# Kernel optimization log

Hardware: AMD Instinct MI355X
Metric: run time of the kernel (lower is better)

Reference implementation:

```python
import jax, jax.numpy as jnp
import numpy as np

D_MODEL = 1024
NUM_HEADS = 16
HEAD_DIM = D_MODEL // NUM_HEADS
FFN_HIDDEN = 4096
EPS = 1e-5


def setup_inputs() -> dict:
    key = jax.random.key(0)
    ks = jax.random.split(key, 7)
    s = 0.02
    return {
        "x": jax.random.normal(ks[0], (2, 2048, D_MODEL), dtype=jnp.float32),
        "W_qkv": jax.random.normal(ks[1], (D_MODEL, 3 * D_MODEL), dtype=jnp.float32) * s,
        "b_qkv": jnp.zeros((3 * D_MODEL,), dtype=jnp.float32),
        "W_o": jax.random.normal(ks[2], (D_MODEL, D_MODEL), dtype=jnp.float32) * s,
        "b_o": jnp.zeros((D_MODEL,), dtype=jnp.float32),
        "gamma1": jnp.ones((D_MODEL,), dtype=jnp.float32),
        "beta1": jnp.zeros((D_MODEL,), dtype=jnp.float32),
        "W1": jax.random.normal(ks[3], (D_MODEL, FFN_HIDDEN), dtype=jnp.float32) * s,
        "b1": jnp.zeros((FFN_HIDDEN,), dtype=jnp.float32),
        "W2": jax.random.normal(ks[4], (FFN_HIDDEN, D_MODEL), dtype=jnp.float32) * s,
        "b2": jnp.zeros((D_MODEL,), dtype=jnp.float32),
        "gamma2": jnp.ones((D_MODEL,), dtype=jnp.float32),
        "beta2": jnp.zeros((D_MODEL,), dtype=jnp.float32),
    }


def _layernorm(x, gamma, beta):
    mean = jnp.mean(x, axis=-1, keepdims=True)
    var = jnp.mean((x - mean) ** 2, axis=-1, keepdims=True)
    return gamma * (x - mean) / jnp.sqrt(var + EPS) + beta


def reference(x, W_qkv, b_qkv, W_o, b_o, gamma1, beta1, W1, b1, W2, b2, gamma2, beta2):
    B, S, D = x.shape
    # ---- multi-head attention ----
    qkv = x @ W_qkv + b_qkv                       # [B,S,3D]
    qkv = qkv.reshape(B, S, NUM_HEADS, 3 * HEAD_DIM).transpose(0, 2, 1, 3)  # [B,H,S,3hd]
    q, k, v = jnp.split(qkv, 3, axis=-1)          # each [B,H,S,hd]
    scores = jnp.einsum("bhqd,bhkd->bhqk", q, k) / np.sqrt(HEAD_DIM)
    attn = jax.nn.softmax(scores, axis=-1)
    vals = jnp.einsum("bhqk,bhkd->bhqd", attn, v)
    vals = vals.transpose(0, 2, 1, 3).reshape(B, S, D)
    attn_out = vals @ W_o + b_o
    # dropout disabled (eval mode)
    h = _layernorm(attn_out + x, gamma1, beta1)
    # ---- position-wise FFN (dropout before relu per source, disabled) ----
    ffn = jax.nn.relu(h @ W1 + b1) @ W2 + b2
    return _layernorm(ffn + h, gamma2, beta2)
```

## Files before the change

### kernel.cpp

```cpp
#include <hip/hip_runtime.h>
#include <stdint.h>

typedef float v4f __attribute__((ext_vector_type(4)));
typedef __bf16 v8bf __attribute__((ext_vector_type(8)));
typedef __bf16 v4bf __attribute__((ext_vector_type(4)));
typedef unsigned short v8us __attribute__((ext_vector_type(8)));
typedef unsigned short v4us __attribute__((ext_vector_type(4)));

__device__ __forceinline__ float b2f(unsigned short u) {
    union { float f; uint32_t i; } x; x.i = ((uint32_t)u) << 16; return x.f;
}
__device__ __forceinline__ unsigned short f2b(float f) {
    union { float f; uint32_t u; } x; x.f = f;
    uint32_t r = x.u + 0x7fffu + ((x.u >> 16) & 1u);
    return (unsigned short)(r >> 16);
}

__device__ __forceinline__ void gload16(const unsigned short* g, unsigned short* l) {
    __builtin_amdgcn_global_load_lds(
        (const __attribute__((address_space(1))) void*)g,
        (__attribute__((address_space(3))) void*)l,
        16, 0, 0);
}

__global__ __launch_bounds__(256) void convert_f32_bf16(
    const float* __restrict__ src, unsigned short* __restrict__ dst)
{
    int i = (blockIdx.x * 256 + threadIdx.x) * 4;
    float4 v = *(const float4*)&src[i];
    v4us o = {f2b(v.x), f2b(v.y), f2b(v.z), f2b(v.w)};
    *(v4us*)&dst[i] = o;
}

__global__ __launch_bounds__(256) void transpose_to_bt(
    const float* __restrict__ W, unsigned short* __restrict__ WT, int K, int N)
{
    __shared__ unsigned short t[64][65];
    const int kb = blockIdx.y * 64, nb = blockIdx.x * 64;
    const int r = threadIdx.x >> 4, c4 = (threadIdx.x & 15) * 4;
    #pragma unroll
    for (int i = 0; i < 4; ++i) {
        int k = r + i * 16;
        float4 v = *(const float4*)&W[(size_t)(kb + k) * N + nb + c4];
        t[c4 + 0][k] = f2b(v.x);
        t[c4 + 1][k] = f2b(v.y);
        t[c4 + 2][k] = f2b(v.z);
        t[c4 + 3][k] = f2b(v.w);
    }
    __syncthreads();
    #pragma unroll
    for (int i = 0; i < 4; ++i) {
        int n = r + i * 16;
        v4us o = {t[n][c4], t[n][c4 + 1], t[n][c4 + 2], t[n][c4 + 3]};
        *(v4us*)&WT[(size_t)(nb + n) * K + kb + c4] = o;
    }
}

__device__ __forceinline__ void xcd_swizzle(int& bm, int& bn) {
    int NB = gridDim.x, MB = gridDim.y;
    int flat = blockIdx.x + NB * blockIdx.y;
    int xcd = flat & 7, j = flat >> 3;
    int MBand = MB >> 3;
    bm = xcd * MBand + (j % MBand);
    bn = j / MBand;
}

template<int SPLIT_V>
__global__ __launch_bounds__(256) void gemm_bt(
    const unsigned short* __restrict__ A, const unsigned short* __restrict__ BT,
    const float* __restrict__ bias, unsigned short* __restrict__ C,
    unsigned short* __restrict__ VT, int M, int N, int K, int relu)
{
    __shared__ __align__(16) unsigned short sA[2][128 * 32];
    __shared__ __align__(16) unsigned short sB[2][128 * 32];
    const int tid  = threadIdx.x;
    const int wave = tid >> 6, lane = tid & 63;
    const int wm = wave >> 1, wn = wave & 1;
    const int quad = lane >> 4, l16 = lane & 15;
    int bm, bn;
    xcd_swizzle(bm, bn);

    const int srow = lane >> 2, scol = (lane & 3) * 8;
    const unsigned short* ga0 = A  + (size_t)(bm * 128 + (wave * 2 + 0) * 16 + srow) * K + scol;
    const unsigned short* ga1 = A  + (size_t)(bm * 128 + (wave * 2 + 1) * 16 + srow) * K + scol;
    const unsigned short* gb0 = BT + (size_t)(bn * 128 + (wave * 2 + 0) * 16 + srow) * K + scol;
    const unsigned short* gb1 = BT + (size_t)(bn * 128 + (wave * 2 + 1) * 16 + srow) * K + scol;
    const int o0 = (wave * 2 + 0) * 512 + lane * 8;
    const int o1 = (wave * 2 + 1) * 512 + lane * 8;

    v8us aR[2][2], bR[2][2];
    #pragma unroll
    for (int c = 0; c < 2; ++c) {
        aR[c][0] = *(const v8us*)(ga0 + c * 32);
        aR[c][1] = *(const v8us*)(ga1 + c * 32);
        bR[c][0] = *(const v8us*)(gb0 + c * 32);
        bR[c][1] = *(const v8us*)(gb1 + c * 32);
    }

    v4f acc[4][4];
    #pragma unroll
    for (int i = 0; i < 4; ++i)
        #pragma unroll
        for (int j = 0; j < 4; ++j)
            acc[i][j] = (v4f){0.f, 0.f, 0.f, 0.f};

    for (int kt = 0; kt < K; kt += 64) {
        __syncthreads();
        #pragma unroll
        for (int c = 0; c < 2; ++c) {
            *(v8us*)&sA[c][o0] = aR[c][0];
            *(v8us*)&sA[c][o1] = aR[c][1];
            *(v8us*)&sB[c][o0] = bR[c][0];
            *(v8us*)&sB[c][o1] = bR[c][1];
        }
        __syncthreads();
        if (kt + 64 < K) {
            int kn = kt + 64;
            #pragma unroll
            for (int c = 0; c < 2; ++c) {
                aR[c][0] = *(const v8us*)(ga0 + kn + c * 32);
                aR[c][1] = *(const v8us*)(ga1 + kn + c * 32);
                bR[c][0] = *(const v8us*)(gb0 + kn + c * 32);
                bR[c][1] = *(const v8us*)(gb1 + kn + c * 32);
            }
        }

        #pragma unroll
        for (int c = 0; c < 2; ++c) {
            v8bf af[4], bfr[4];
            #pragma unroll
            for (int mt = 0; mt < 4; ++mt)
                af[mt] = *(const v8bf*)&sA[c][(wm * 64 + mt * 16 + l16) * 32 + quad * 8];
            #pragma unroll
            for (int nt = 0; nt < 4; ++nt)
                bfr[nt] = *(const v8bf*)&sB[c][(wn * 64 + nt * 16 + l16) * 32 + quad * 8];
            #pragma unroll
            for (int mt = 0; mt < 4; ++mt)
                #pragma unroll
                for (int nt = 0; nt < 4; ++nt)
                    acc[mt][nt] = __builtin_amdgcn_mfma_f32_16x16x32_bf16(
                        af[mt], bfr[nt], acc[mt][nt], 0, 0, 0);
        }
    }

    #pragma unroll
    for (int mt = 0; mt < 4; ++mt) {
        int row = bm * 128 + wm * 64 + mt * 16 + quad * 4;
        #pragma unroll
        for (int nt = 0; nt < 4; ++nt) {
            int c0 = bn * 128 + wn * 64 + nt * 16;
            int col = c0 + l16;
            float bv = bias ? bias[col] : 0.f;
            if (SPLIT_V && (c0 % 192) >= 128) {
                int hh = c0 / 192;
                int d  = (c0 % 192) - 128 + l16;
                int bb = row >> 11;
                int s  = row & 2047;
                v4us st;
                #pragma unroll
                for (int r = 0; r < 4; ++r)
                    st[r] = f2b(acc[mt][nt][r] + bv);
                *(v4us*)&VT[((size_t)(bb * 16 + hh) * 64 + d) * 2048 + s] = st;
            } else {
                float qs = (SPLIT_V && (c0 % 192) < 64) ? 0.18033688f : 1.0f;
                #pragma unroll
                for (int r = 0; r < 4; ++r) {
                    float v = (acc[mt][nt][r] + bv) * qs;
                    if (relu) v = fmaxf(v, 0.f);
                    C[(size_t)(row + r) * N + col] = f2b(v);
                }
            }
        }
    }
}

__global__ __launch_bounds__(256) void gemm_bt_n64(
    const unsigned short* __restrict__ A, const unsigned short* __restrict__ BT,
    const float* __restrict__ bias, unsigned short* __restrict__ C,
    int M, int N, int K, int relu)
{
    __shared__ __align__(16) unsigned short sA[2][128 * 32];
    __shared__ __align__(16) unsigned short sB[2][64 * 32];
    const int tid  = threadIdx.x;
    const int wave = tid >> 6, lane = tid & 63;
    const int wm = wave >> 1, wn = wave & 1;
    const int quad = lane >> 4, l16 = lane & 15;
    int bm, bn;
    xcd_swizzle(bm, bn);

    const int srow = lane >> 2, scol = (lane & 3) * 8;
    const unsigned short* ga0 = A  + (size_t)(bm * 128 + (wave * 2 + 0) * 16 + srow) * K + scol;
    const unsigned short* ga1 = A  + (size_t)(bm * 128 + (wave * 2 + 1) * 16 + srow) * K + scol;
    const unsigned short* gb0 = BT + (size_t)(bn * 64 + wave * 16 + srow) * K + scol;
    const int oa0 = (wave * 2 + 0) * 512 + lane * 8;
    const int oa1 = (wave * 2 + 1) * 512 + lane * 8;
    const int ob  = wave * 512 + lane * 8;

    v8us aR[2][2], bR[2];
    #pragma unroll
    for (int c = 0; c < 2; ++c) {
        aR[c][0] = *(const v8us*)(ga0 + c * 32);
        aR[c][1] = *(const v8us*)(ga1 + c * 32);
        bR[c]    = *(const v8us*)(gb0 + c * 32);
    }

    v4f acc[4][2];
    #pragma unroll
    for (int i = 0; i < 4; ++i)
        #pragma unroll
        for (int j = 0; j < 2; ++j)
            acc[i][j] = (v4f){0.f, 0.f, 0.f, 0.f};

    for (int kt = 0; kt < K; kt += 64) {
        __syncthreads();
        #pragma unroll
        for (int c = 0; c < 2; ++c) {
            *(v8us*)&sA[c][oa0] = aR[c][0];
            *(v8us*)&sA[c][oa1] = aR[c][1];
            *(v8us*)&sB[c][ob]  = bR[c];
        }
        __syncthreads();
        if (kt + 64 < K) {
            int kn = kt + 64;
            #pragma unroll
            for (int c = 0; c < 2; ++c) {
                aR[c][0] = *(const v8us*)(ga0 + kn + c * 32);
                aR[c][1] = *(const v8us*)(ga1 + kn + c * 32);
                bR[c]    = *(const v8us*)(gb0 + kn + c * 32);
            }
        }

        #pragma unroll
        for (int c = 0; c < 2; ++c) {
            v8bf af[4], bfr[2];
            #pragma unroll
            for (int mt = 0; mt < 4; ++mt)
                af[mt] = *(const v8bf*)&sA[c][(wm * 64 + mt * 16 + l16) * 32 + quad * 8];
            #pragma unroll
            for (int nt = 0; nt < 2; ++nt)
                bfr[nt] = *(const v8bf*)&sB[c][(wn * 32 + nt * 16 + l16) * 32 + quad * 8];
            #pragma unroll
            for (int mt = 0; mt < 4; ++mt)
                #pragma unroll
                for (int nt = 0; nt < 2; ++nt)
                    acc[mt][nt] = __builtin_amdgcn_mfma_f32_16x16x32_bf16(
                        af[mt], bfr[nt], acc[mt][nt], 0, 0, 0);
        }
    }

    #pragma unroll
    for (int mt = 0; mt < 4; ++mt) {
        #pragma unroll
        for (int nt = 0; nt < 2; ++nt) {
            int col = bn * 64 + wn * 32 + nt * 16 + l16;
            float bv = bias ? bias[col] : 0.f;
            #pragma unroll
            for (int r = 0; r < 4; ++r) {
                int row = bm * 128 + wm * 64 + mt * 16 + quad * 4 + r;
                float v = acc[mt][nt][r] + bv;
                if (relu) v = fmaxf(v, 0.f);
                C[(size_t)row * N + col] = f2b(v);
            }
        }
    }
}

__global__ __launch_bounds__(512) void gemm256(
    const unsigned short* __restrict__ A, const unsigned short* __restrict__ BT,
    const float* __restrict__ bias, unsigned short* __restrict__ C,
    int M, int N, int K, int relu)
{
    __shared__ __align__(16) unsigned short sA[2][256 * 64];
    __shared__ __align__(16) unsigned short sB[2][256 * 64];
    const int tid  = threadIdx.x;
    const int wave = tid >> 6, lane = tid & 63;
    const int wm = wave >> 2, wn = wave & 3;
    const int quad = lane >> 4, l16 = lane & 15;
    int bm, bn;
    xcd_swizzle(bm, bn);

    const int srow = lane >> 3;
    const int scol = ((lane & 7) * 8) ^ ((lane & 32) ? 16 : 0);
    size_t aoff[4], boff[4];
    #pragma unroll
    for (int j = 0; j < 4; ++j) {
        int r = wave * 32 + j * 8 + srow;
        aoff[j] = (size_t)(bm * 256 + r) * K + scol;
        boff[j] = (size_t)(bn * 256 + r) * K + scol;
    }
    const int lds0 = wave * 32 * 64;

    const int ksw = (quad * 8) ^ ((l16 & 4) ? 16 : 0);

    v4f acc[8][4];
    #pragma unroll
    for (int i = 0; i < 8; ++i)
        #pragma unroll
        for (int j = 0; j < 4; ++j)
            acc[i][j] = (v4f){0.f, 0.f, 0.f, 0.f};

    const int NT = K >> 6;
    #pragma unroll
    for (int j = 0; j < 4; ++j) {
        gload16(A  + aoff[j], &sA[0][lds0 + j * 512]);
        gload16(BT + boff[j], &sB[0][lds0 + j * 512]);
    }
    __syncthreads();

    for (int t = 0; t < NT; ++t) {
        const int buf = t & 1;
        if (t + 1 < NT) {
            const int ktn = (t + 1) << 6;
            #pragma unroll
            for (int j = 0; j < 4; ++j) {
                gload16(A  + aoff[j] + ktn, &sA[buf ^ 1][lds0 + j * 512]);
                gload16(BT + boff[j] + ktn, &sB[buf ^ 1][lds0 + j * 512]);
            }
        }

        v8bf bfr[4][2];
        #pragma unroll
        for (int nt2 = 0; nt2 < 4; ++nt2)
            #pragma unroll
            for (int kc = 0; kc < 2; ++kc)
                bfr[nt2][kc] = *(const v8bf*)&sB[buf][
                    (wn * 64 + nt2 * 16 + l16) * 64 + kc * 32 + ksw];
        #pragma unroll
        for (int mq = 0; mq < 2; ++mq) {
            v8bf af[4][2];
            #pragma unroll
            for (int mt2 = 0; mt2 < 4; ++mt2)
                #pragma unroll
                for (int kc = 0; kc < 2; ++kc)
                    af[mt2][kc] = *(const v8bf*)&sA[buf][
                        (wm * 128 + mq * 64 + mt2 * 16 + l16) * 64 + kc * 32 + ksw];
            #pragma unroll
            for (int mt2 = 0; mt2 < 4; ++mt2)
                #pragma unroll
                for (int nt2 = 0; nt2 < 4; ++nt2)
                    #pragma unroll
                    for (int kc = 0; kc < 2; ++kc)
                        acc[mq * 4 + mt2][nt2] =
                            __builtin_amdgcn_mfma_f32_16x16x32_bf16(
                                af[mt2][kc], bfr[nt2][kc],
                                acc[mq * 4 + mt2][nt2], 0, 0, 0);
        }
        __syncthreads();
    }

    #pragma unroll
    for (int mt = 0; mt < 8; ++mt) {
        int row = bm * 256 + wm * 128 + mt * 16 + quad * 4;
        #pragma unroll
        for (int nt = 0; nt < 4; ++nt) {
            int col = bn * 256 + wn * 64 + nt * 16 + l16;
            float bv = bias ? bias[col] : 0.f;
            #pragma unroll
            for (int r = 0; r < 4; ++r) {
                float v = acc[mt][nt][r] + bv;
                if (relu) v = fmaxf(v, 0.f);
                C[(size_t)(row + r) * N + col] = f2b(v);
            }
        }
    }
}

__global__ __launch_bounds__(512) void attn_mfma(
    const unsigned short* __restrict__ qkv, const unsigned short* __restrict__ VT,
    unsigned short* __restrict__ av)
{
    __shared__ __align__(16) unsigned short sK[64 * 72];
    __shared__ __align__(16) unsigned short sVT[64 * 72];
    __shared__ __align__(16) unsigned short sP[8][16 * 72];
    const int tid  = threadIdx.x;
    const int wave = tid >> 6, lane = tid & 63;
    const int quad = lane >> 4, l16 = lane & 15;
    const int blk = blockIdx.x;
    const int xcd = blk & 7, local = blk >> 3;
    const int bh = xcd * 4 + (local & 3);
    const int qb = local >> 2;
    const int h = bh & 15, b = bh >> 4;
    const int row0 = b * 2048;
    const int qbase = row0 + qb * 128 + wave * 16;
    const size_t qoff = (size_t)h * 192;
    const size_t koff = qoff + 64;

    v8bf qf[2];
    #pragma unroll
    for (int kc = 0; kc < 2; ++kc)
        qf[kc] = *(const v8bf*)&qkv[(size_t)(qbase + l16) * 3072
                                    + qoff + kc * 32 + quad * 8];

    v4f o[4];
    #pragma unroll
    for (int dt = 0; dt < 4; ++dt)
        o[dt] = (v4f){0.f, 0.f, 0.f, 0.f};
    float ll = 0.f;

    const int k_key = tid >> 3, k_oct = (tid & 7) * 8;
    const unsigned short* gK = qkv + (size_t)(row0 + k_key) * 3072 + koff + k_oct;
    const unsigned short* gV = VT + ((size_t)bh * 64 + k_key) * 2048 + k_oct;
    const size_t stepK = (size_t)64 * 3072;
    const size_t stepV = 64;

    v8us kreg = *(const v8us*)gK;
    v8us vreg = *(const v8us*)gV;
    gK += stepK; gV += stepV;

    for (int kt = 0; kt < 32; ++kt) {
        __syncthreads();
        *(v8us*)&sK[k_key * 72 + k_oct]  = kreg;
        *(v8us*)&sVT[k_key * 72 + k_oct] = vreg;
        __syncthreads();
        if (kt < 31) {
            kreg = *(const v8us*)gK;
            vreg = *(const v8us*)gV;
            gK += stepK; gV += stepV;
        }

        v4f sc[4];
        #pragma unroll
        for (int kk = 0; kk < 4; ++kk) {
            sc[kk] = (v4f){0.f, 0.f, 0.f, 0.f};
            #pragma unroll
            for (int kc = 0; kc < 2; ++kc) {
                v8bf ak = *(const v8bf*)&sK[(kk * 16 + l16) * 72 + kc * 32 + quad * 8];
                sc[kk] = __builtin_amdgcn_mfma_f32_16x16x32_bf16(
                    ak, qf[kc], sc[kk], 0, 0, 0);
            }
        }

        float ps = 0.f;
        #pragma unroll
        for (int kk = 0; kk < 4; ++kk) {
            v4bf pk;
            #pragma unroll
            for (int rr = 0; rr < 4; ++rr) {
                float p = __builtin_amdgcn_exp2f(sc[kk][rr]);
                ps += p;
                pk[rr] = (__bf16)p;
            }
            *(v4bf*)&sP[wave][l16 * 72 + kk * 16 + quad * 4] = pk;
        }
        ll += ps;

        __asm__ volatile("s_waitcnt lgkmcnt(0)" ::: "memory");

        #pragma unroll
        for (int c = 0; c < 2; ++c) {
            union { v8bf v; v8us u; } u;
            u.u = *(const v8us*)&sP[wave][l16 * 72 + c * 32 + quad * 8];
            v8bf pb = u.v;
            #pragma unroll
            for (int dt = 0; dt < 4; ++dt) {
                v8bf va = *(const v8bf*)&sVT[(dt * 16 + l16) * 72 + c * 32 + quad * 8];
                o[dt] = __builtin_amdgcn_mfma_f32_16x16x32_bf16(
                    va, pb, o[dt], 0, 0, 0);
            }
        }
    }

    float l = ll;
    l += __shfl_xor(l, 16, 64);
    l += __shfl_xor(l, 32, 64);
    float inv = 1.f / l;
    int qrow = qbase + l16;
    #pragma unroll
    for (int dt = 0; dt < 4; ++dt) {
        v4bf st;
        #pragma unroll
        for (int rr = 0; rr < 4; ++rr)
            st[rr] = (__bf16)(o[dt][rr] * inv);
        *(v4bf*)&av[(size_t)qrow * 1024 + h * 64 + dt * 16 + quad * 4] = st;
    }
}

template<int RES_F32, int OUT_F32>
__global__ __launch_bounds__(256) void ln_fused(
    const unsigned short* __restrict__ a, const void* __restrict__ residv,
    const float* __restrict__ gamma, const float* __restrict__ beta,
    void* __restrict__ outv)
{
    const int row = blockIdx.x, tid = threadIdx.x;
    const size_t base = (size_t)row * 1024;
    const int c0 = tid * 4;
    ushort4 avv = *(const ushort4*)&a[base + c0];
    float y[4];
    if (RES_F32) {
        float4 rv = *(const float4*)((const float*)residv + base + c0);
        y[0] = b2f(avv.x) + rv.x;
        y[1] = b2f(avv.y) + rv.y;
        y[2] = b2f(avv.z) + rv.z;
        y[3] = b2f(avv.w) + rv.w;
    } else {
        ushort4 rv = *(const ushort4*)((const unsigned short*)residv + base + c0);
        y[0] = b2f(avv.x) + b2f(rv.x);
        y[1] = b2f(avv.y) + b2f(rv.y);
        y[2] = b2f(avv.z) + b2f(rv.z);
        y[3] = b2f(avv.w) + b2f(rv.w);
    }
    float s  = y[0] + y[1] + y[2] + y[3];
    float ss = y[0]*y[0] + y[1]*y[1] + y[2]*y[2] + y[3]*y[3];
    #pragma unroll
    for (int off = 32; off; off >>= 1) {
        s  += __shfl_xor(s, off, 64);
        ss += __shfl_xor(ss, off, 64);
    }
    __shared__ float red[8];
    int wave = tid >> 6, lane = tid & 63;
    if (lane == 0) { red[wave] = s; red[4 + wave] = ss; }
    __syncthreads();
    s  = red[0] + red[1] + red[2] + red[3];
    ss = red[4] + red[5] + red[6] + red[7];
    float mean = s * (1.f / 1024.f);
    float var  = ss * (1.f / 1024.f) - mean * mean;
    float rstd = rsqrtf(var + 1e-5f);
    float4 gv = *(const float4*)&gamma[c0];
    float4 bv = *(const float4*)&beta[c0];
    float r0 = gv.x * (y[0] - mean) * rstd + bv.x;
    float r1 = gv.y * (y[1] - mean) * rstd + bv.y;
    float r2 = gv.z * (y[2] - mean) * rstd + bv.z;
    float r3 = gv.w * (y[3] - mean) * rstd + bv.w;
    if (OUT_F32) {
        float4 ov = {r0, r1, r2, r3};
        *(float4*)((float*)outv + base + c0) = ov;
    } else {
        ushort4 ov;
        ov.x = f2b(r0); ov.y = f2b(r1); ov.z = f2b(r2); ov.w = f2b(r3);
        *(ushort4*)((unsigned short*)outv + base + c0) = ov;
    }
}

extern "C" void kernel_launch(void* const* d_in, const int* in_sizes, int n_in,
                              void* d_out, int out_size, void* d_ws, size_t ws_size,
                              hipStream_t stream)
{
    (void)in_sizes; (void)n_in; (void)out_size; (void)ws_size;
    const float* x    = (const float*)d_in[0];
    const float* Wqkv = (const float*)d_in[1];
    const float* bqkv = (const float*)d_in[2];
    const float* Wo   = (const float*)d_in[3];
    const float* bo   = (const float*)d_in[4];
    const float* g1   = (const float*)d_in[5];
    const float* be1  = (const float*)d_in[6];
    const float* W1   = (const float*)d_in[7];
    const float* b1   = (const float*)d_in[8];
    const float* W2   = (const float*)d_in[9];
    const float* b2   = (const float*)d_in[10];
    const float* g2   = (const float*)d_in[11];
    const float* be2  = (const float*)d_in[12];
    float* out = (float*)d_out;

    unsigned short* R0 = (unsigned short*)d_ws;
    unsigned short* R1 = R0 + (size_t)16 * 1024 * 1024;
    unsigned short* R2 = R1 + (size_t)4 * 1024 * 1024;
    unsigned short* R3 = R2 + (size_t)4 * 1024 * 1024;
    unsigned short* WqkvT = R0 + (size_t)12 * 1024 * 1024;

    const int M = 4096;
    dim3 blk(256);

    convert_f32_bf16<<<dim3(M * 1024 / 1024), blk, 0, stream>>>(x, R2);
    transpose_to_bt<<<dim3(48, 16), blk, 0, stream>>>(Wqkv, WqkvT, 1024, 3072);
    gemm_bt<1><<<dim3(24, 32), blk, 0, stream>>>(R2, WqkvT, bqkv, R0, R1, M, 3072, 1024, 0);
    attn_mfma<<<dim3(512), dim3(512), 0, stream>>>(R0, R1, R3);
    transpose_to_bt<<<dim3(16, 16), blk, 0, stream>>>(Wo, R2, 1024, 1024);
    gemm_bt_n64<<<dim3(16, 32), blk, 0, stream>>>(R3, R2, bo, R1, M, 1024, 1024, 0);
    ln_fused<1, 0><<<dim3(4096), blk, 0, stream>>>(R1, x, g1, be1, R2);
    transpose_to_bt<<<dim3(64, 16), blk, 0, stream>>>(W1, R3, 1024, 4096);
    gemm256<<<dim3(16, 16), dim3(512), 0, stream>>>(R2, R3, b1, R0, M, 4096, 1024, 1);
    transpose_to_bt<<<dim3(16, 64), blk, 0, stream>>>(W2, R1, 4096, 1024);
    gemm_bt_n64<<<dim3(16, 32), blk, 0, stream>>>(R0, R1, b2, R3, M, 1024, 4096, 0);
    ln_fused<0, 1><<<dim3(4096), blk, 0, stream>>>(R3, R2, g2, be2, out);
}
```

Measured before the change: 350.0 us.

## Use 256x256 gemm for QKV projection and double-buffer K/V tiles in attention

The QKV projection moves from the 128x128 register-staged gemm_bt kernel to the 256x256 gemm256 kernel, which loads straight into LDS through global_load_lds. gemm256 gains a SPLIT_V template parameter so it can still write V transposed and scale Q. The attention kernel double-buffers its K/V LDS tiles, which removes one __syncthreads per key tile. The QKV grid becomes 12x16=192 blocks, fewer than the CU count, which may leave some CUs idle. Doubling the attention LDS footprint may reduce occupancy.

```diff
diff --git a/kernel.cpp b/kernel.cpp
--- a/kernel.cpp
+++ b/kernel.cpp
@@ -65,14 +65,13 @@
     bn = j / MBand;
 }
 
-template<int SPLIT_V>
-__global__ __launch_bounds__(256) void gemm_bt(
+__global__ __launch_bounds__(256) void gemm_bt_n64(
     const unsigned short* __restrict__ A, const unsigned short* __restrict__ BT,
     const float* __restrict__ bias, unsigned short* __restrict__ C,
-    unsigned short* __restrict__ VT, int M, int N, int K, int relu)
+    int M, int N, int K, int relu)
 {
     __shared__ __align__(16) unsigned short sA[2][128 * 32];
-    __shared__ __align__(16) unsigned short sB[2][128 * 32];
+    __shared__ __align__(16) unsigned short sB[2][64 * 32];
     const int tid  = threadIdx.x;
     const int wave = tid >> 6, lane = tid & 63;
     const int wm = wave >> 1, wn = wave & 1;
@@ -83,35 +82,33 @@
     const int srow = lane >> 2, scol = (lane & 3) * 8;
     const unsigned short* ga0 = A  + (size_t)(bm * 128 + (wave * 2 + 0) * 16 + srow) * K + scol;
     const unsigned short* ga1 = A  + (size_t)(bm * 128 + (wave * 2 + 1) * 16 + srow) * K + scol;
-    const unsigned short* gb0 = BT + (size_t)(bn * 128 + (wave * 2 + 0) * 16 + srow) * K + scol;
-    const unsigned short* gb1 = BT + (size_t)(bn * 128 + (wave * 2 + 1) * 16 + srow) * K + scol;
-    const int o0 = (wave * 2 + 0) * 512 + lane * 8;
-    const int o1 = (wave * 2 + 1) * 512 + lane * 8;
-
-    v8us aR[2][2], bR[2][2];
+    const unsigned short* gb0 = BT + (size_t)(bn * 64 + wave * 16 + srow) * K + scol;
+    const int oa0 = (wave * 2 + 0) * 512 + lane * 8;
+    const int oa1 = (wave * 2 + 1) * 512 + lane * 8;
+    const int ob  = wave * 512 + lane * 8;
+
+    v8us aR[2][2], bR[2];
     #pragma unroll
     for (int c = 0; c < 2; ++c) {
         aR[c][0] = *(const v8us*)(ga0 + c * 32);
         aR[c][1] = *(const v8us*)(ga1 + c * 32);
-        bR[c][0] = *(const v8us*)(gb0 + c * 32);
-        bR[c][1] = *(const v8us*)(gb1 + c * 32);
-    }
-
-    v4f acc[4][4];
+        bR[c]    = *(const v8us*)(gb0 + c * 32);
+    }
+
+    v4f acc[4][2];
     #pragma unroll
     for (int i = 0; i < 4; ++i)
         #pragma unroll
-        for (int j = 0; j < 4; ++j)
+        for (int j = 0; j < 2; ++j)
             acc[i][j] = (v4f){0.f, 0.f, 0.f, 0.f};
 
     for (int kt = 0; kt < K; kt += 64) {
         __syncthreads();
         #pragma unroll
         for (int c = 0; c < 2; ++c) {
-            *(v8us*)&sA[c][o0] = aR[c][0];
-            *(v8us*)&sA[c][o1] = aR[c][1];
-            *(v8us*)&sB[c][o0] = bR[c][0];
-            *(v8us*)&sB[c][o1] = bR[c][1];
+            *(v8us*)&sA[c][oa0] = aR[c][0];
+            *(v8us*)&sA[c][oa1] = aR[c][1];
+            *(v8us*)&sB[c][ob]  = bR[c];
         }
         __syncthreads();
         if (kt + 64 < K) {
@@ -120,24 +117,23 @@
             for (int c = 0; c < 2; ++c) {
                 aR[c][0] = *(const v8us*)(ga0 + kn + c * 32);
                 aR[c][1] = *(const v8us*)(ga1 + kn + c * 32);
-                bR[c][0] = *(const v8us*)(gb0 + kn + c * 32);
-                bR[c][1] = *(const v8us*)(gb1 + kn + c * 32);
+                bR[c]    = *(const v8us*)(gb0 + kn + c * 32);
             }
         }
 
         #pragma unroll
         for (int c = 0; c < 2; ++c) {
-            v8bf af[4], bfr[4];
+            v8bf af[4], bfr[2];
             #pragma unroll
             for (int mt = 0; mt < 4; ++mt)
                 af[mt] = *(const v8bf*)&sA[c][(wm * 64 + mt * 16 + l16) * 32 + quad * 8];
             #pragma unroll
-            for (int nt = 0; nt < 4; ++nt)
-                bfr[nt] = *(const v8bf*)&sB[c][(wn * 64 + nt * 16 + l16) * 32 + quad * 8];
+            for (int nt = 0; nt < 2; ++nt)
+                bfr[nt] = *(const v8bf*)&sB[c][(wn * 32 + nt * 16 + l16) * 32 + quad * 8];
             #pragma unroll
             for (int mt = 0; mt < 4; ++mt)
                 #pragma unroll
-                for (int nt = 0; nt < 4; ++nt)
+                for (int nt = 0; nt < 2; ++nt)
                     acc[mt][nt] = __builtin_amdgcn_mfma_f32_16x16x32_bf16(
                         af[mt], bfr[nt], acc[mt][nt], 0, 0, 0);
         }
@@ -145,10 +141,111 @@
 
     #pragma unroll
     for (int mt = 0; mt < 4; ++mt) {
-        int row = bm * 128 + wm * 64 + mt * 16 + quad * 4;
+        #pragma unroll
+        for (int nt = 0; nt < 2; ++nt) {
+            int col = bn * 64 + wn * 32 + nt * 16 + l16;
+            float bv = bias ? bias[col] : 0.f;
+            #pragma unroll
+            for (int r = 0; r < 4; ++r) {
+                int row = bm * 128 + wm * 64 + mt * 16 + quad * 4 + r;
+                float v = acc[mt][nt][r] + bv;
+                if (relu) v = fmaxf(v, 0.f);
+                C[(size_t)row * N + col] = f2b(v);
+            }
+        }
+    }
+}
+
+template<int SPLIT_V>
+__global__ __launch_bounds__(512) void gemm256(
+    const unsigned short* __restrict__ A, const unsigned short* __restrict__ BT,
+    const float* __restrict__ bias, unsigned short* __restrict__ C,
+    unsigned short* __restrict__ VT, int M, int N, int K, int relu)
+{
+    __shared__ __align__(16) unsigned short sA[2][256 * 64];
+    __shared__ __align__(16) unsigned short sB[2][256 * 64];
+    const int tid  = threadIdx.x;
+    const int wave = tid >> 6, lane = tid & 63;
+    const int wm = wave >> 2, wn = wave & 3;
+    const int quad = lane >> 4, l16 = lane & 15;
+    int bm, bn;
+    xcd_swizzle(bm, bn);
+
+    const int srow = lane >> 3;
+    const int scol = ((lane & 7) * 8) ^ ((lane & 32) ? 16 : 0);
+    size_t aoff[4], boff[4];
+    #pragma unroll
+    for (int j = 0; j < 4; ++j) {
+        int r = wave * 32 + j * 8 + srow;
+        aoff[j] = (size_t)(bm * 256 + r) * K + scol;
+        boff[j] = (size_t)(bn * 256 + r) * K + scol;
+    }
+    const int lds0 = wave * 32 * 64;
+
+    const int ksw = (quad * 8) ^ ((l16 & 4) ? 16 : 0);
+
+    v4f acc[8][4];
+    #pragma unroll
+    for (int i = 0; i < 8; ++i)
+        #pragma unroll
+        for (int j = 0; j < 4; ++j)
+            acc[i][j] = (v4f){0.f, 0.f, 0.f, 0.f};
+
+    const int NT = K >> 6;
+    #pragma unroll
+    for (int j = 0; j < 4; ++j) {
+        gload16(A  + aoff[j], &sA[0][lds0 + j * 512]);
+        gload16(BT + boff[j], &sB[0][lds0 + j * 512]);
+    }
+    __syncthreads();
+
+    for (int t = 0; t < NT; ++t) {
+        const int buf = t & 1;
+        if (t + 1 < NT) {
+            const int ktn = (t + 1) << 6;
+            #pragma unroll
+            for (int j = 0; j < 4; ++j) {
+                gload16(A  + aoff[j] + ktn, &sA[buf ^ 1][lds0 + j * 512]);
+                gload16(BT + boff[j] + ktn, &sB[buf ^ 1][lds0 + j * 512]);
+            }
+        }
+
+        v8bf bfr[4][2];
+        #pragma unroll
+        for (int nt2 = 0; nt2 < 4; ++nt2)
+            #pragma unroll
+            for (int kc = 0; kc < 2; ++kc)
+                bfr[nt2][kc] = *(const v8bf*)&sB[buf][
+                    (wn * 64 + nt2 * 16 + l16) * 64 + kc * 32 + ksw];
+        #pragma unroll
+        for (int mq = 0; mq < 2; ++mq) {
+            v8bf af[4][2];
+            #pragma unroll
+            for (int mt2 = 0; mt2 < 4; ++mt2)
+                #pragma unroll
+                for (int kc = 0; kc < 2; ++kc)
+                    af[mt2][kc] = *(const v8bf*)&sA[buf][
+                        (wm * 128 + mq * 64 + mt2 * 16 + l16) * 64 + kc * 32 + ksw];
+            #pragma unroll
+            for (int mt2 = 0; mt2 < 4; ++mt2)
+                #pragma unroll
+                for (int nt2 = 0; nt2 < 4; ++nt2)
+                    #pragma unroll
+                    for (int kc = 0; kc < 2; ++kc)
+                        acc[mq * 4 + mt2][nt2] =
+                            __builtin_amdgcn_mfma_f32_16x16x32_bf16(
+                                af[mt2][kc], bfr[nt2][kc],
+                                acc[mq * 4 + mt2][nt2], 0, 0, 0);
+        }
+        __syncthreads();
+    }
+
+    #pragma unroll
+    for (int mt = 0; mt < 8; ++mt) {
+        int row = bm * 256 + wm * 128 + mt * 16 + quad * 4;
         #pragma unroll
         for (int nt = 0; nt < 4; ++nt) {
-            int c0 = bn * 128 + wn * 64 + nt * 16;
+            int c0 = bn * 256 + wn * 64 + nt * 16;
             int col = c0 + l16;
             float bv = bias ? bias[col] : 0.f;
             if (SPLIT_V && (c0 % 192) >= 128) {
@@ -174,203 +271,12 @@
     }
 }
 
-__global__ __launch_bounds__(256) void gemm_bt_n64(
-    const unsigned short* __restrict__ A, const unsigned short* __restrict__ BT,
-    const float* __restrict__ bias, unsigned short* __restrict__ C,
-    int M, int N, int K, int relu)
-{
-    __shared__ __align__(16) unsigned short sA[2][128 * 32];
-    __shared__ __align__(16) unsigned short sB[2][64 * 32];
-    const int tid  = threadIdx.x;
-    const int wave = tid >> 6, lane = tid & 63;
-    const int wm = wave >> 1, wn = wave & 1;
-    const int quad = lane >> 4, l16 = lane & 15;
-    int bm, bn;
-    xcd_swizzle(bm, bn);
-
-    const int srow = lane >> 2, scol = (lane & 3) * 8;
-    const unsigned short* ga0 = A  + (size_t)(bm * 128 + (wave * 2 + 0) * 16 + srow) * K + scol;
-    const unsigned short* ga1 = A  + (size_t)(bm * 128 + (wave * 2 + 1) * 16 + srow) * K + scol;
-    const unsigned short* gb0 = BT + (size_t)(bn * 64 + wave * 16 + srow) * K + scol;
-    const int oa0 = (wave * 2 + 0) * 512 + lane * 8;
-    const int oa1 = (wave * 2 + 1) * 512 + lane * 8;
-    const int ob  = wave * 512 + lane * 8;
-
-    v8us aR[2][2], bR[2];
-    #pragma unroll
-    for (int c = 0; c < 2; ++c) {
-        aR[c][0] = *(const v8us*)(ga0 + c * 32);
-        aR[c][1] = *(const v8us*)(ga1 + c * 32);
-        bR[c]    = *(const v8us*)(gb0 + c * 32);
-    }
-
-    v4f acc[4][2];
-    #pragma unroll
-    for (int i = 0; i < 4; ++i)
-        #pragma unroll
-        for (int j = 0; j < 2; ++j)
-            acc[i][j] = (v4f){0.f, 0.f, 0.f, 0.f};
-
-    for (int kt = 0; kt < K; kt += 64) {
-        __syncthreads();
-        #pragma unroll
-        for (int c = 0; c < 2; ++c) {
-            *(v8us*)&sA[c][oa0] = aR[c][0];
-            *(v8us*)&sA[c][oa1] = aR[c][1];
-            *(v8us*)&sB[c][ob]  = bR[c];
-        }
-        __syncthreads();
-        if (kt + 64 < K) {
-            int kn = kt + 64;
-            #pragma unroll
-            for (int c = 0; c < 2; ++c) {
-                aR[c][0] = *(const v8us*)(ga0 + kn + c * 32);
-                aR[c][1] = *(const v8us*)(ga1 + kn + c * 32);
-                bR[c]    = *(const v8us*)(gb0 + kn + c * 32);
-            }
-        }
-
-        #pragma unroll
-        for (int c = 0; c < 2; ++c) {
-            v8bf af[4], bfr[2];
-            #pragma unroll
-            for (int mt = 0; mt < 4; ++mt)
-                af[mt] = *(const v8bf*)&sA[c][(wm * 64 + mt * 16 + l16) * 32 + quad * 8];
-            #pragma unroll
-            for (int nt = 0; nt < 2; ++nt)
-                bfr[nt] = *(const v8bf*)&sB[c][(wn * 32 + nt * 16 + l16) * 32 + quad * 8];
-            #pragma unroll
-            for (int mt = 0; mt < 4; ++mt)
-                #pragma unroll
-                for (int nt = 0; nt < 2; ++nt)
-                    acc[mt][nt] = __builtin_amdgcn_mfma_f32_16x16x32_bf16(
-                        af[mt], bfr[nt], acc[mt][nt], 0, 0, 0);
-        }
-    }
-
-    #pragma unroll
-    for (int mt = 0; mt < 4; ++mt) {
-        #pragma unroll
-        for (int nt = 0; nt < 2; ++nt) {
-            int col = bn * 64 + wn * 32 + nt * 16 + l16;
-            float bv = bias ? bias[col] : 0.f;
-            #pragma unroll
-            for (int r = 0; r < 4; ++r) {
-                int row = bm * 128 + wm * 64 + mt * 16 + quad * 4 + r;
-                float v = acc[mt][nt][r] + bv;
-                if (relu) v = fmaxf(v, 0.f);
-                C[(size_t)row * N + col] = f2b(v);
-            }
-        }
-    }
-}
-
-__global__ __launch_bounds__(512) void gemm256(
-    const unsigned short* __restrict__ A, const unsigned short* __restrict__ BT,
-    const float* __restrict__ bias, unsigned short* __restrict__ C,
-    int M, int N, int K, int relu)
-{
-    __shared__ __align__(16) unsigned short sA[2][256 * 64];
-    __shared__ __align__(16) unsigned short sB[2][256 * 64];
-    const int tid  = threadIdx.x;
-    const int wave = tid >> 6, lane = tid & 63;
-    const int wm = wave >> 2, wn = wave & 3;
-    const int quad = lane >> 4, l16 = lane & 15;
-    int bm, bn;
-    xcd_swizzle(bm, bn);
-
-    const int srow = lane >> 3;
-    const int scol = ((lane & 7) * 8) ^ ((lane & 32) ? 16 : 0);
-    size_t aoff[4], boff[4];
-    #pragma unroll
-    for (int j = 0; j < 4; ++j) {
-        int r = wave * 32 + j * 8 + srow;
-        aoff[j] = (size_t)(bm * 256 + r) * K + scol;
-        boff[j] = (size_t)(bn * 256 + r) * K + scol;
-    }
-    const int lds0 = wave * 32 * 64;
-
-    const int ksw = (quad * 8) ^ ((l16 & 4) ? 16 : 0);
-
-    v4f acc[8][4];
-    #pragma unroll
-    for (int i = 0; i < 8; ++i)
-        #pragma unroll
-        for (int j = 0; j < 4; ++j)
-            acc[i][j] = (v4f){0.f, 0.f, 0.f, 0.f};
-
-    const int NT = K >> 6;
-    #pragma unroll
-    for (int j = 0; j < 4; ++j) {
-        gload16(A  + aoff[j], &sA[0][lds0 + j * 512]);
-        gload16(BT + boff[j], &sB[0][lds0 + j * 512]);
-    }
-    __syncthreads();
-
-    for (int t = 0; t < NT; ++t) {
-        const int buf = t & 1;
-        if (t + 1 < NT) {
-            const int ktn = (t + 1) << 6;
-            #pragma unroll
-            for (int j = 0; j < 4; ++j) {
-                gload16(A  + aoff[j] + ktn, &sA[buf ^ 1][lds0 + j * 512]);
-                gload16(BT + boff[j] + ktn, &sB[buf ^ 1][lds0 + j * 512]);
-            }
-        }
-
-        v8bf bfr[4][2];
-        #pragma unroll
-        for (int nt2 = 0; nt2 < 4; ++nt2)
-            #pragma unroll
-            for (int kc = 0; kc < 2; ++kc)
-                bfr[nt2][kc] = *(const v8bf*)&sB[buf][
-                    (wn * 64 + nt2 * 16 + l16) * 64 + kc * 32 + ksw];
-        #pragma unroll
-        for (int mq = 0; mq < 2; ++mq) {
-            v8bf af[4][2];
-            #pragma unroll
-            for (int mt2 = 0; mt2 < 4; ++mt2)
-                #pragma unroll
-                for (int kc = 0; kc < 2; ++kc)
-                    af[mt2][kc] = *(const v8bf*)&sA[buf][
-                        (wm * 128 + mq * 64 + mt2 * 16 + l16) * 64 + kc * 32 + ksw];
-            #pragma unroll
-            for (int mt2 = 0; mt2 < 4; ++mt2)
-                #pragma unroll
-                for (int nt2 = 0; nt2 < 4; ++nt2)
-                    #pragma unroll
-                    for (int kc = 0; kc < 2; ++kc)
-                        acc[mq * 4 + mt2][nt2] =
-                            __builtin_amdgcn_mfma_f32_16x16x32_bf16(
-                                af[mt2][kc], bfr[nt2][kc],
-                                acc[mq * 4 + mt2][nt2], 0, 0, 0);
-        }
-        __syncthreads();
-    }
-
-    #pragma unroll
-    for (int mt = 0; mt < 8; ++mt) {
-        int row = bm * 256 + wm * 128 + mt * 16 + quad * 4;
-        #pragma unroll
-        for (int nt = 0; nt < 4; ++nt) {
-            int col = bn * 256 + wn * 64 + nt * 16 + l16;
-            float bv = bias ? bias[col] : 0.f;
-            #pragma unroll
-            for (int r = 0; r < 4; ++r) {
-                float v = acc[mt][nt][r] + bv;
-                if (relu) v = fmaxf(v, 0.f);
-                C[(size_t)(row + r) * N + col] = f2b(v);
-            }
-        }
-    }
-}
-
 __global__ __launch_bounds__(512) void attn_mfma(
     const unsigned short* __restrict__ qkv, const unsigned short* __restrict__ VT,
     unsigned short* __restrict__ av)
 {
-    __shared__ __align__(16) unsigned short sK[64 * 72];
-    __shared__ __align__(16) unsigned short sVT[64 * 72];
+    __shared__ __align__(16) unsigned short sK[2][64 * 72];
+    __shared__ __align__(16) unsigned short sVT[2][64 * 72];
     __shared__ __align__(16) unsigned short sP[8][16 * 72];
     const int tid  = threadIdx.x;
     const int wave = tid >> 6, lane = tid & 63;
@@ -408,9 +314,9 @@
     gK += stepK; gV += stepV;
 
     for (int kt = 0; kt < 32; ++kt) {
-        __syncthreads();
-        *(v8us*)&sK[k_key * 72 + k_oct]  = kreg;
-        *(v8us*)&sVT[k_key * 72 + k_oct] = vreg;
+        const int cur = kt & 1;
+        *(v8us*)&sK[cur][k_key * 72 + k_oct]  = kreg;
+        *(v8us*)&sVT[cur][k_key * 72 + k_oct] = vreg;
         __syncthreads();
         if (kt < 31) {
             kreg = *(const v8us*)gK;
@@ -424,7 +330,7 @@
             sc[kk] = (v4f){0.f, 0.f, 0.f, 0.f};
             #pragma unroll
             for (int kc = 0; kc < 2; ++kc) {
-                v8bf ak = *(const v8bf*)&sK[(kk * 16 + l16) * 72 + kc * 32 + quad * 8];
+                v8bf ak = *(const v8bf*)&sK[cur][(kk * 16 + l16) * 72 + kc * 32 + quad * 8];
                 sc[kk] = __builtin_amdgcn_mfma_f32_16x16x32_bf16(
                     ak, qf[kc], sc[kk], 0, 0, 0);
             }
@@ -453,7 +359,7 @@
             v8bf pb = u.v;
             #pragma unroll
             for (int dt = 0; dt < 4; ++dt) {
-                v8bf va = *(const v8bf*)&sVT[(dt * 16 + l16) * 72 + c * 32 + quad * 8];
+                v8bf va = *(const v8bf*)&sVT[cur][(dt * 16 + l16) * 72 + c * 32 + quad * 8];
                 o[dt] = __builtin_amdgcn_mfma_f32_16x16x32_bf16(
                     va, pb, o[dt], 0, 0, 0);
             }
@@ -562,13 +468,13 @@
 
     convert_f32_bf16<<<dim3(M * 1024 / 1024), blk, 0, stream>>>(x, R2);
     transpose_to_bt<<<dim3(48, 16), blk, 0, stream>>>(Wqkv, WqkvT, 1024, 3072);
-    gemm_bt<1><<<dim3(24, 32), blk, 0, stream>>>(R2, WqkvT, bqkv, R0, R1, M, 3072, 1024, 0);
+    gemm256<1><<<dim3(12, 16), dim3(512), 0, stream>>>(R2, WqkvT, bqkv, R0, R1, M, 3072, 1024, 0);
     attn_mfma<<<dim3(512), dim3(512), 0, stream>>>(R0, R1, R3);
     transpose_to_bt<<<dim3(16, 16), blk, 0, stream>>>(Wo, R2, 1024, 1024);
     gemm_bt_n64<<<dim3(16, 32), blk, 0, stream>>>(R3, R2, bo, R1, M, 1024, 1024, 0);
     ln_fused<1, 0><<<dim3(4096), blk, 0, stream>>>(R1, x, g1, be1, R2);
     transpose_to_bt<<<dim3(64, 16), blk, 0, stream>>>(W1, R3, 1024, 4096);
-    gemm256<<<dim3(16, 16), dim3(512), 0, stream>>>(R2, R3, b1, R0, M, 4096, 1024, 1);
+    gemm256<0><<<dim3(16, 16), dim3(512), 0, stream>>>(R2, R3, b1, R0, nullptr, M, 4096, 1024, 1);
     transpose_to_bt<<<dim3(16, 64), blk, 0, stream>>>(W2, R1, 4096, 1024);
     gemm_bt_n64<<<dim3(16, 32), blk, 0, stream>>>(R0, R1, b2, R3, M, 1024, 4096, 0);
     ln_fused<0, 1><<<dim3(4096), blk, 0, stream>>>(R3, R2, g2, be2, out);
```

New measurement: 348.5 us. Within noise of the previous version (-0.4%).
